# Kernel optimization log

Measured on AMD Instinct MI355X. Metric: run time of the kernel, lower is better.

Reference implementation:

```python
import jax, jax.numpy as jnp
import numpy as np
import math

B, S, D = 4, 1024, 1024
H, DK = 16, 64
NUM_BUCKETS, MAX_DIST = 32, 128


def _relative_position_bucket(relative_position, num_buckets=NUM_BUCKETS, max_distance=MAX_DIST):
    # bidirectional bucketing (T5 encoder style)
    num_buckets = num_buckets // 2
    buckets = (relative_position > 0).astype(jnp.int32) * num_buckets
    rp = jnp.abs(relative_position)
    max_exact = num_buckets // 2
    is_small = rp < max_exact
    # clamp to >=1 to avoid log(0); masked out by is_small anyway
    rp_large = max_exact + (
        jnp.log(jnp.maximum(rp, 1).astype(jnp.float32) / max_exact)
        / math.log(max_distance / max_exact)
        * (num_buckets - max_exact)
    ).astype(jnp.int32)
    rp_large = jnp.minimum(rp_large, num_buckets - 1)
    return buckets + jnp.where(is_small, rp, rp_large)


def compute_bias(rel_bias_table, q_len, k_len):
    ctx = jnp.arange(q_len)[:, None]
    mem = jnp.arange(k_len)[None, :]
    buckets = _relative_position_bucket(mem - ctx)  # [q,k]
    values = rel_bias_table[buckets]  # [q,k,H]
    return jnp.transpose(values, (2, 0, 1))  # [H,q,k]


def setup_inputs() -> dict:
    key = jax.random.key(0)
    ks = jax.random.split(key, 6)
    return {
        "hidden_states": jax.random.normal(ks[0], (B, S, D), dtype=jnp.float32),
        "Wq": jax.random.normal(ks[1], (D, H * DK), dtype=jnp.float32) * 0.02,
        "Wk": jax.random.normal(ks[2], (D, H * DK), dtype=jnp.float32) * 0.02,
        "Wv": jax.random.normal(ks[3], (D, H * DK), dtype=jnp.float32) * 0.02,
        "Wo": jax.random.normal(ks[4], (H * DK, D), dtype=jnp.float32) * 0.02,
        "rel_bias_table": jax.random.normal(ks[5], (NUM_BUCKETS, H), dtype=jnp.float32),
    }


def reference(hidden_states, Wq, Wk, Wv, Wo, rel_bias_table):
    b, s, _ = hidden_states.shape
    # projections (no bias), split heads -> [b,h,s,dk]
    def heads(x):
        return jnp.transpose(x.reshape(b, s, H, DK), (0, 2, 1, 3))
    q = heads(hidden_states @ Wq)
    k = heads(hidden_states @ Wk)
    v = heads(hidden_states @ Wv)
    # NOTE: T5 attention is UNSCALED (no 1/sqrt(dk))
    scores = jnp.einsum("bhqd,bhkd->bhqk", q, k)
    bias = compute_bias(rel_bias_table, s, s)[None]  # [1,H,s,s]
    scores = scores + bias
    attn = jax.nn.softmax(scores.astype(jnp.float32), axis=-1).astype(scores.dtype)
    out = jnp.einsum("bhqk,bhkd->bhqd", attn, v)
    out = jnp.transpose(out, (0, 2, 1, 3)).reshape(b, s, H * DK)
    return out @ Wo
```

## Files before the change

kernel.cpp:

```cpp
#include <hip/hip_runtime.h>
#include <hip/hip_bf16.h>

typedef __attribute__((ext_vector_type(8))) short short8;
typedef __attribute__((ext_vector_type(4))) float f32x4;
typedef unsigned short u16;

#define AS1 __attribute__((address_space(1)))
#define AS3 __attribute__((address_space(3)))

#define LOG2E 1.44269504088896f
#define FOLD_M 46.166241308446828f
#define EXP2(x) __builtin_amdgcn_exp2f(x)

__device__ __forceinline__ u16 f2bf(float f) {
    unsigned u = __builtin_bit_cast(unsigned, f);
    u += 0x7FFFu + ((u >> 16) & 1u);
    return (u16)(u >> 16);
}

__device__ __forceinline__ unsigned pk2(float a, float b) {
    unsigned ua = __builtin_bit_cast(unsigned, a) + 0x8000u;
    unsigned ub = __builtin_bit_cast(unsigned, b) + 0x8000u;
    return __builtin_amdgcn_perm(ub, ua, 0x07060302);
}

__global__ __launch_bounds__(256) void k_prep(const float* __restrict__ hidden,
                                              const float* __restrict__ Wq, const float* __restrict__ Wk,
                                              const float* __restrict__ Wv, const float* __restrict__ Wo,
                                              const float* __restrict__ tbl,
                                              u16* __restrict__ hidb,
                                              u16* __restrict__ wt, u16* __restrict__ wot,
                                              float* __restrict__ bias2) {
    int z = blockIdx.z;
    if (z >= 5) {
        int i = ((z - 5) * 1024 + blockIdx.y * 32 + blockIdx.x) * 256 + threadIdx.x;
        float4 v = ((const float4*)hidden)[i];
        ushort4 o;
        o.x = f2bf(v.x); o.y = f2bf(v.y); o.z = f2bf(v.z); o.w = f2bf(v.w);
        ((ushort4*)hidb)[i] = o;
        return;
    }
    if (z == 4) {
        int idx = (blockIdx.y * 32 + blockIdx.x) * 256 + threadIdx.x;
        if (idx < 16 * 2048) {
            int r = idx & 2047, h = idx >> 11;
            int rel = r - 1023;
            int bucket = rel > 0 ? 16 : 0;
            int rp = rel < 0 ? -rel : rel;
            if (rp < 8) bucket += rp;
            else {
                int lb = 8 + (int)(log2f((float)rp * 0.125f) * 2.0f);
                bucket += (lb < 15 ? lb : 15);
            }
            bias2[idx] = tbl[bucket * 16 + h] * LOG2E - FOLD_M;
        }
        return;
    }
    const float* in = z == 0 ? Wq : z == 1 ? Wk : z == 2 ? Wv : Wo;
    u16* out = (z == 3) ? wot : wt + (size_t)z * 1024 * 1024;
    __shared__ float tile[32][33];
    int tx = threadIdx.x & 31, ty = threadIdx.x >> 5;
    int bx = blockIdx.x << 5, by = blockIdx.y << 5;
    #pragma unroll
    for (int j = 0; j < 32; j += 8)
        tile[ty + j][tx] = in[(size_t)(by + ty + j) * 1024 + bx + tx];
    __syncthreads();
    #pragma unroll
    for (int j = 0; j < 32; j += 8)
        out[(size_t)(bx + ty + j) * 1024 + by + tx] = f2bf(tile[tx][ty + j]);
}

template<int MODE, int FM>
__global__ __launch_bounds__(256) void k_gemm(const u16* __restrict__ A, const u16* __restrict__ Bt,
                                              u16* __restrict__ oq, u16* __restrict__ ok,
                                              u16* __restrict__ ov, float* __restrict__ outf,
                                              int N) {
    const int K = 1024;
    __shared__ u16 As[2][FM * 1024];
    __shared__ u16 Bs[2][4096];
    int t = threadIdx.x, lane = t & 63, wave = t >> 6;
    int m0 = blockIdx.y * (FM * 32), n0 = blockIdx.x << 7;
    int wm = (wave >> 1) * (FM * 16), wn = (wave & 1) << 6;
    int g = lane >> 4, ln = lane & 15;
    f32x4 acc[FM][4];
    #pragma unroll
    for (int i = 0; i < FM; i++)
        #pragma unroll
        for (int j = 0; j < 4; j++) acc[i][j] = (f32x4){0.f, 0.f, 0.f, 0.f};

    int schunk = ((lane & 3) ^ ((lane >> 3) & 3)) << 3;
    const u16* gA = A + (size_t)(m0 + wave * 16 + (lane >> 2)) * K + schunk;
    const u16* gB = Bt + (size_t)(n0 + wave * 16 + (lane >> 2)) * K + schunk;
    int ldsOff = wave * 512;

    #define GSTAGE(k0_, buf_)                                                                          \
        {                                                                                              \
            __builtin_amdgcn_global_load_lds((const AS1 void*)(gA + (k0_)),                            \
                                             (AS3 void*)&As[buf_][ldsOff], 16, 0, 0);                  \
            if (FM == 4)                                                                               \
                __builtin_amdgcn_global_load_lds((const AS1 void*)(gA + 64 * K + (k0_)),               \
                                                 (AS3 void*)&As[buf_][ldsOff + 2048], 16, 0, 0);       \
            __builtin_amdgcn_global_load_lds((const AS1 void*)(gB + (k0_)),                            \
                                             (AS3 void*)&Bs[buf_][ldsOff], 16, 0, 0);                  \
            __builtin_amdgcn_global_load_lds((const AS1 void*)(gB + 64 * K + (k0_)),                   \
                                             (AS3 void*)&Bs[buf_][ldsOff + 2048], 16, 0, 0);           \
        }

    GSTAGE(0, 0);
    __syncthreads();

    int rchunk = (g ^ ((ln >> 1) & 3)) << 3;

    #pragma unroll 2
    for (int kb = 0; kb < 32; kb++) {
        const int cur = kb & 1;
        if (kb < 31) GSTAGE((kb + 1) * 32, cur ^ 1);

        short8 af[FM], bfr[4];
        #pragma unroll
        for (int fm = 0; fm < FM; fm++)
            af[fm] = *(const short8*)&As[cur][(wm + (fm << 4) + ln) * 32 + rchunk];
        #pragma unroll
        for (int fn = 0; fn < 4; fn++)
            bfr[fn] = *(const short8*)&Bs[cur][(wn + (fn << 4) + ln) * 32 + rchunk];
        #pragma unroll
        for (int fm = 0; fm < FM; fm++)
            #pragma unroll
            for (int fn = 0; fn < 4; fn++)
                acc[fm][fn] = __builtin_amdgcn_mfma_f32_16x16x32_bf16(af[fm], bfr[fn], acc[fm][fn], 0, 0, 0);

        __syncthreads();
    }

    #pragma unroll
    for (int fm = 0; fm < FM; fm++)
        #pragma unroll
        for (int fn = 0; fn < 4; fn++) {
            int mb = m0 + wm + (fm << 4) + (g << 2);
            int n = n0 + wn + (fn << 4) + ln;
            if (MODE == 0) {
                int j = n >> 10, col = n & 1023;
                int h = col >> 6, dk = col & 63;
                int b = mb >> 10, s = mb & 1023;
                if (j == 2) {
                    ushort4 pk;
                    pk.x = f2bf(acc[fm][fn][0]); pk.y = f2bf(acc[fm][fn][1]);
                    pk.z = f2bf(acc[fm][fn][2]); pk.w = f2bf(acc[fm][fn][3]);
                    *(ushort4*)(ov + ((size_t)(((b << 4) + h) * 64 + dk)) * 1024 + s) = pk;
                } else {
                    u16* dst = (j == 0) ? oq : ok;
                    #pragma unroll
                    for (int r = 0; r < 4; r++)
                        dst[((size_t)(((b << 4) + h) * 1024 + s + r)) * 64 + dk] = f2bf(acc[fm][fn][r]);
                }
            } else {
                #pragma unroll
                for (int r = 0; r < 4; r++)
                    outf[(size_t)(mb + r) * N + n] = acc[fm][fn][r];
            }
        }
    #undef GSTAGE
}

__global__ __launch_bounds__(256, 2) void k_attn(const u16* __restrict__ Qg, const u16* __restrict__ Kg,
                                                 const u16* __restrict__ Vtg, const float* __restrict__ bias2,
                                                 u16* __restrict__ attn_out) {
    __shared__ __align__(16) u16 Ks[2][64 * 64];
    __shared__ __align__(16) u16 Vts[2][64 * 64];
    __shared__ __align__(16) u16 Ps[128 * 64];
    __shared__ __align__(16) float blds4[4][1160];

    int t = threadIdx.x, lane = t & 63, w = t >> 6;
    int bid = blockIdx.x;
    int sid = (bid & 7) * 64 + (bid >> 3);
    int qb = sid & 7, h = (sid >> 3) & 15, b = sid >> 7;
    int q0 = qb << 7;
    const u16* Qh = Qg + ((size_t)(((b << 4) + h) * 1024 + q0)) * 64;
    const u16* Kh = Kg + (size_t)(((b << 4) + h)) * 1024 * 64;
    const u16* Vth = Vtg + (size_t)(((b << 4) + h)) * 64 * 1024;
    const float* bh = bias2 + (h << 11);

    int g = lane >> 4, ln = lane & 15;
    int swz = (ln & 7) << 4;

    short8 qf[2][2];
    #pragma unroll
    for (int fm = 0; fm < 2; fm++)
        #pragma unroll
        for (int kh = 0; kh < 2; kh++)
            qf[fm][kh] = *(const short8*)(Qh + (size_t)(w * 32 + fm * 16 + ln) * 64 + kh * 32 + g * 8);

    int w0 = 896 - q0;
    for (int i = t; i < 1152; i += 256) {
        float v = bh[w0 + i];
        #pragma unroll
        for (int a2 = 0; a2 < 4; a2++) { int x = i - a2; if (x >= 0) blds4[a2][x] = v; }
    }
    float b_hi = bh[1023 + 256];
    float b_lo = bh[1023 - 256];
    int aRep = (3 - ln) & 3;
    const float* repB = &blds4[aRep][0];

    #define STAGE(kb_, buf_)                                                                     \
        {                                                                                        \
            _Pragma("unroll")                                                                    \
            for (int r2 = 0; r2 < 2; r2++) {                                                     \
                int L = t * 16 + r2 * 4096;                                                      \
                int row = L >> 7, gI = (L >> 4) & 7, gp = gI ^ (row & 7);                        \
                __builtin_amdgcn_global_load_lds(                                                \
                    (const AS1 void*)(Kh + (size_t)((kb_) * 64 + row) * 64 + gp * 8),            \
                    (AS3 void*)&Ks[buf_][L >> 1], 16, 0, 0);                                     \
                __builtin_amdgcn_global_load_lds(                                                \
                    (const AS1 void*)(Vth + (size_t)row * 1024 + (kb_) * 64 + gp * 8),           \
                    (AS3 void*)&Vts[buf_][L >> 1], 16, 0, 0);                                    \
            }                                                                                    \
        }

    STAGE(0, 0);
    __syncthreads();

    float psum[2] = {0.f, 0.f};
    f32x4 o[2][4];
    #pragma unroll
    for (int fm = 0; fm < 2; fm++)
        #pragma unroll
        for (int dn = 0; dn < 4; dn++) o[fm][dn] = (f32x4){0.f, 0.f, 0.f, 0.f};

    #pragma unroll 2
    for (int kb = 0; kb < 16; kb++) {
        const int cur = kb & 1;
        if (kb < 15) STAGE(kb + 1, cur ^ 1);

        f32x4 s[2][4];
        __builtin_amdgcn_s_setprio(1);
        #pragma unroll
        for (int fn = 0; fn < 4; fn++) {
            int row = (fn << 4) + ln;
            short8 kf0 = *(const short8*)((const char*)Ks[cur] + row * 128 + (((g << 4) + 0)  ^ ((row & 7) << 4)));
            short8 kf1 = *(const short8*)((const char*)Ks[cur] + row * 128 + (((g << 4) + 64) ^ ((row & 7) << 4)));
            #pragma unroll
            for (int fm = 0; fm < 2; fm++) {
                f32x4 a = (f32x4){0.f, 0.f, 0.f, 0.f};
                a = __builtin_amdgcn_mfma_f32_16x16x32_bf16(kf0, qf[fm][0], a, 0, 0, 0);
                a = __builtin_amdgcn_mfma_f32_16x16x32_bf16(kf1, qf[fm][1], a, 0, 0, 0);
                s[fm][fn] = a;
            }
        }
        __builtin_amdgcn_s_setprio(0);

        int d0 = 64 * kb - q0 - 32 * w;
        int ibase = 64 * kb - 32 * w + 127 + 4 * g - ln;
        bool fast = (d0 >= 122) || (d0 <= -154);
        float bu = d0 > 0 ? b_hi : b_lo;
        #pragma unroll
        for (int fm = 0; fm < 2; fm++) {
            int prow = 32 * w + 16 * fm + ln;
            #pragma unroll
            for (int fn = 0; fn < 4; fn++) {
                f32x4 sv = s[fm][fn];
                float b0, b1, b2v, b3;
                if (fast) { b0 = b1 = b2v = b3 = bu; }
                else {
                    float4 bb = *(const float4*)(repB + (ibase + 16 * fn - 16 * fm - aRep));
                    b0 = bb.x; b1 = bb.y; b2v = bb.z; b3 = bb.w;
                }
                float p0 = EXP2(fmaf(sv[0], LOG2E, b0));
                float p1 = EXP2(fmaf(sv[1], LOG2E, b1));
                float p2 = EXP2(fmaf(sv[2], LOG2E, b2v));
                float p3 = EXP2(fmaf(sv[3], LOG2E, b3));
                psum[fm] += (p0 + p1) + (p2 + p3);
                uint2 pv;
                pv.x = pk2(p0, p1);
                pv.y = pk2(p2, p3);
                *(uint2*)((char*)Ps + prow * 128 + (((fn << 5) + (g << 3)) ^ swz)) = pv;
            }
        }

        short8 pa[2][2];
        #pragma unroll
        for (int fm = 0; fm < 2; fm++) {
            int prow = 32 * w + 16 * fm + ln;
            #pragma unroll
            for (int kh = 0; kh < 2; kh++)
                pa[fm][kh] = *(const short8*)((const char*)Ps + prow * 128 + (((kh << 6) + (g << 4)) ^ swz));
        }
        __builtin_amdgcn_s_setprio(1);
        #pragma unroll
        for (int dn = 0; dn < 4; dn++) {
            int vrow = (dn << 4) + ln;
            short8 vb0 = *(const short8*)((const char*)Vts[cur] + vrow * 128 + (((g << 4) + 0)  ^ ((vrow & 7) << 4)));
            short8 vb1 = *(const short8*)((const char*)Vts[cur] + vrow * 128 + (((g << 4) + 64) ^ ((vrow & 7) << 4)));
            #pragma unroll
            for (int fm = 0; fm < 2; fm++) {
                f32x4 a = o[fm][dn];
                a = __builtin_amdgcn_mfma_f32_16x16x32_bf16(pa[fm][0], vb0, a, 0, 0, 0);
                a = __builtin_amdgcn_mfma_f32_16x16x32_bf16(pa[fm][1], vb1, a, 0, 0, 0);
                o[fm][dn] = a;
            }
        }
        __builtin_amdgcn_s_setprio(0);

        __syncthreads();
    }

    float linv[2][4];
    #pragma unroll
    for (int fm = 0; fm < 2; fm++) {
        float v = psum[fm];
        v += __shfl_xor(v, 16);
        v += __shfl_xor(v, 32);
        float inv = 1.0f / v;
        #pragma unroll
        for (int r = 0; r < 4; r++)
            linv[fm][r] = __shfl(inv, 4 * g + r);
    }
    #pragma unroll
    for (int fm = 0; fm < 2; fm++)
        #pragma unroll
        for (int dn = 0; dn < 4; dn++)
            #pragma unroll
            for (int r = 0; r < 4; r++) {
                int srow = q0 + 32 * w + 16 * fm + (g << 2) + r;
                int col = (h << 6) + (dn << 4) + ln;
                attn_out[((size_t)((b << 10) + srow) << 10) + col] = f2bf(o[fm][dn][r] * linv[fm][r]);
            }
}

extern "C" void kernel_launch(void* const* d_in, const int* in_sizes, int n_in,
                              void* d_out, int out_size, void* d_ws, size_t ws_size,
                              hipStream_t stream) {
    const float* hidden = (const float*)d_in[0];
    const float* Wq = (const float*)d_in[1];
    const float* Wk = (const float*)d_in[2];
    const float* Wv = (const float*)d_in[3];
    const float* Wo = (const float*)d_in[4];
    const float* tbl = (const float*)d_in[5];

    u16* hidb = (u16*)d_ws;
    u16* wt   = hidb + 4096 * 1024;
    u16* wot  = wt + 3072 * 1024;
    u16* Qb   = wot + 1024 * 1024;
    u16* Kb   = Qb + 4 * 16 * 1024 * 64;
    u16* Vb   = Kb + 4 * 16 * 1024 * 64;
    u16* attn = Vb + 4 * 16 * 1024 * 64;
    float* bias = (float*)(attn + 4096 * 1024);

    k_prep<<<dim3(32, 32, 9), 256, 0, stream>>>(hidden, Wq, Wk, Wv, Wo, tbl, hidb, wt, wot, bias);
    k_gemm<0, 4><<<dim3(24, 32), 256, 0, stream>>>(hidb, wt, Qb, Kb, Vb, nullptr, 3072);
    k_attn<<<512, 256, 0, stream>>>(Qb, Kb, Vb, bias, attn);
    k_gemm<1, 2><<<dim3(8, 64), 256, 0, stream>>>(attn, wot, nullptr, nullptr, nullptr,
                                                  (float*)d_out, 1024);
}
```

Measured before the change: 102.9 us.

## Keep attention probabilities in registers via permlane32 swap; swizzle GEMM block order

The attention kernel stops writing the softmax probabilities to a shared-memory tile and reading them back. Instead it permutes the K rows used for the QK^T MFMA so that each lane's packed probabilities can be rearranged into PV operand layout with v_permlane32_swap. This removes the LDS store/load round trip and frees the Ps buffer, which may raise occupancy. Separately, the GEMM remaps block IDs so neighbouring blocks land in groups of eight, aiming for better L2 locality. The register permutation depends on an exact lane mapping and on hardware-specific inline assembly, so any mismatch would produce wrong results.

Measured after the change: 96.79 us. 1.06x faster.

```diff
diff --git a/kernel.cpp b/kernel.cpp
--- a/kernel.cpp
+++ b/kernel.cpp
@@ -3,6 +3,7 @@
 
 typedef __attribute__((ext_vector_type(8))) short short8;
 typedef __attribute__((ext_vector_type(4))) float f32x4;
+typedef __attribute__((ext_vector_type(4))) unsigned u32x4;
 typedef unsigned short u16;
 
 #define AS1 __attribute__((address_space(1)))
@@ -76,10 +77,14 @@
                                               u16* __restrict__ ov, float* __restrict__ outf,
                                               int N) {
     const int K = 1024;
+    const int GX = (MODE == 0) ? 24 : 8;
+    const int NWG = (MODE == 0) ? 768 : 512;
     __shared__ u16 As[2][FM * 1024];
     __shared__ u16 Bs[2][4096];
     int t = threadIdx.x, lane = t & 63, wave = t >> 6;
-    int m0 = blockIdx.y * (FM * 32), n0 = blockIdx.x << 7;
+    int bid = blockIdx.y * GX + blockIdx.x;
+    int sbid = (bid & 7) * (NWG / 8) + (bid >> 3);
+    int m0 = (sbid / GX) * (FM * 32), n0 = (sbid % GX) << 7;
     int wm = (wave >> 1) * (FM * 16), wn = (wave & 1) << 6;
     int g = lane >> 4, ln = lane & 15;
     f32x4 acc[FM][4];
@@ -167,7 +172,6 @@
                                                  u16* __restrict__ attn_out) {
     __shared__ __align__(16) u16 Ks[2][64 * 64];
     __shared__ __align__(16) u16 Vts[2][64 * 64];
-    __shared__ __align__(16) u16 Ps[128 * 64];
     __shared__ __align__(16) float blds4[4][1160];
 
     int t = threadIdx.x, lane = t & 63, w = t >> 6;
@@ -181,7 +185,8 @@
     const float* bh = bias2 + (h << 11);
 
     int g = lane >> 4, ln = lane & 15;
-    int swz = (ln & 7) << 4;
+    int lnk = (ln & 3) | ((ln & 4) << 1) | ((ln & 8) >> 1);
+    int kbq = ((g & 1) << 3) | ((g >> 1) << 2);
 
     short8 qf[2][2];
     #pragma unroll
@@ -235,7 +240,7 @@
         __builtin_amdgcn_s_setprio(1);
         #pragma unroll
         for (int fn = 0; fn < 4; fn++) {
-            int row = (fn << 4) + ln;
+            int row = (fn << 4) + lnk;
             short8 kf0 = *(const short8*)((const char*)Ks[cur] + row * 128 + (((g << 4) + 0)  ^ ((row & 7) << 4)));
             short8 kf1 = *(const short8*)((const char*)Ks[cur] + row * 128 + (((g << 4) + 64) ^ ((row & 7) << 4)));
             #pragma unroll
@@ -249,12 +254,12 @@
         __builtin_amdgcn_s_setprio(0);
 
         int d0 = 64 * kb - q0 - 32 * w;
-        int ibase = 64 * kb - 32 * w + 127 + 4 * g - ln;
+        int ibase = 64 * kb - 32 * w + 127 + kbq - ln;
         bool fast = (d0 >= 122) || (d0 <= -154);
         float bu = d0 > 0 ? b_hi : b_lo;
-        #pragma unroll
-        for (int fm = 0; fm < 2; fm++) {
-            int prow = 32 * w + 16 * fm + ln;
+        unsigned Px[2][4], Py[2][4];
+        #pragma unroll
+        for (int fm = 0; fm < 2; fm++)
             #pragma unroll
             for (int fn = 0; fn < 4; fn++) {
                 f32x4 sv = s[fm][fn];
@@ -269,21 +274,23 @@
                 float p2 = EXP2(fmaf(sv[2], LOG2E, b2v));
                 float p3 = EXP2(fmaf(sv[3], LOG2E, b3));
                 psum[fm] += (p0 + p1) + (p2 + p3);
-                uint2 pv;
-                pv.x = pk2(p0, p1);
-                pv.y = pk2(p2, p3);
-                *(uint2*)((char*)Ps + prow * 128 + (((fn << 5) + (g << 3)) ^ swz)) = pv;
-            }
-        }
+                Px[fm][fn] = pk2(p0, p1);
+                Py[fm][fn] = pk2(p2, p3);
+            }
 
         short8 pa[2][2];
         #pragma unroll
-        for (int fm = 0; fm < 2; fm++) {
-            int prow = 32 * w + 16 * fm + ln;
-            #pragma unroll
-            for (int kh = 0; kh < 2; kh++)
-                pa[fm][kh] = *(const short8*)((const char*)Ps + prow * 128 + (((kh << 6) + (g << 4)) ^ swz));
-        }
+        for (int fm = 0; fm < 2; fm++)
+            #pragma unroll
+            for (int ks = 0; ks < 2; ks++) {
+                unsigned w0r = Px[fm][2 * ks], w2r = Px[fm][2 * ks + 1];
+                unsigned w1r = Py[fm][2 * ks], w3r = Py[fm][2 * ks + 1];
+                asm volatile("s_nop 1\n\tv_permlane32_swap_b32 %0, %1" : "+v"(w0r), "+v"(w2r));
+                asm volatile("s_nop 1\n\tv_permlane32_swap_b32 %0, %1" : "+v"(w1r), "+v"(w3r));
+                u32x4 tv; tv[0] = w0r; tv[1] = w1r; tv[2] = w2r; tv[3] = w3r;
+                pa[fm][ks] = __builtin_bit_cast(short8, tv);
+            }
+
         __builtin_amdgcn_s_setprio(1);
         #pragma unroll
         for (int dn = 0; dn < 4; dn++) {
```
